# Performance work log

Hardware: AMD Instinct MI355X
Metric: run time of the kernel (lower is better)

Reference implementation:

```python
import jax, jax.numpy as jnp
import numpy as np

QK_DIM = 1024
V_DIM = 1024
NUM_HEADS = 16
HEAD_DIM = 64
INNER = NUM_HEADS * HEAD_DIM  # 1024
SCALE = HEAD_DIM ** -0.5


def setup_inputs() -> dict:
    key = jax.random.key(0)
    ks = jax.random.split(key, 8)
    m, nq, nkv = 4, 2048, 2048
    xq = jax.random.normal(ks[0], (m, nq, QK_DIM), dtype=jnp.float32)
    xk = jax.random.normal(ks[1], (m, nkv, QK_DIM), dtype=jnp.float32)
    xv = jax.random.normal(ks[2], (m, nkv, V_DIM), dtype=jnp.float32)
    # torch nn.Linear weights are [out, in]; y = x @ W.T
    s_qk = (QK_DIM) ** -0.5
    s_in = (INNER) ** -0.5
    Wq = jax.random.uniform(ks[3], (INNER, QK_DIM), jnp.float32, -s_qk, s_qk)
    Wk = jax.random.uniform(ks[4], (INNER, QK_DIM), jnp.float32, -s_qk, s_qk)
    Wv = jax.random.uniform(ks[5], (INNER, V_DIM), jnp.float32, -s_qk, s_qk)
    Wo = jax.random.uniform(ks[6], (V_DIM, INNER), jnp.float32, -s_in, s_in)
    bo = jax.random.uniform(ks[7], (V_DIM,), jnp.float32, -s_in, s_in)
    return {"xq": xq, "xk": xk, "xv": xv, "Wq": Wq, "Wk": Wk, "Wv": Wv, "Wo": Wo, "bo": bo}


def reference(xq, xk, xv, Wq, Wk, Wv, Wo, bo):
    m, nq, _ = xq.shape
    nkv = xk.shape[1]
    # projections (no bias), split heads: b n (h d) -> b h n d
    q = (xq @ Wq.T).reshape(m, nq, NUM_HEADS, HEAD_DIM).transpose(0, 2, 1, 3)
    k = (xk @ Wk.T).reshape(m, nkv, NUM_HEADS, HEAD_DIM).transpose(0, 2, 1, 3)
    v = (xv @ Wv.T).reshape(m, nkv, NUM_HEADS, HEAD_DIM).transpose(0, 2, 1, 3)
    dots = jnp.einsum("bhqd,bhkd->bhqk", q, k) * SCALE  # [m,h,nq,nkv]
    attn = jax.nn.softmax(dots, axis=-1)
    out = jnp.einsum("bhqk,bhkd->bhqd", attn, v)
    out = out.transpose(0, 2, 1, 3).reshape(m, nq, INNER)  # b h n d -> b n (h d)
    return out @ Wo.T + bo  # to_out Linear (dropout p=0 -> identity)
```

## Files before the change

kernel.cpp:

```cpp
#include <hip/hip_runtime.h>

typedef unsigned short u16;
using bf16x8 = __attribute__((ext_vector_type(8))) __bf16;
using f32x4  = __attribute__((ext_vector_type(4))) float;

#define QSCALE 0.18033688011f

#define EXP2F(x) __builtin_amdgcn_exp2f(x)
#define SCHED_FENCE() __builtin_amdgcn_sched_barrier(0)

__device__ __forceinline__ u16 f2bf(float f) {
  union { float f; unsigned int u; } x; x.f = f;
  unsigned int r = x.u + 0x7FFFu + ((x.u >> 16) & 1u);
  return (u16)(r >> 16);
}

__device__ __forceinline__ bf16x8 ld8(const u16* p) {
  return *reinterpret_cast<const bf16x8*>(p);
}

__device__ __forceinline__ void gload16(const void* g, void* l) {
  __builtin_amdgcn_global_load_lds(
      (const __attribute__((address_space(1))) unsigned int*)g,
      (__attribute__((address_space(3))) unsigned int*)l, 16, 0, 0);
}

__global__ void cast4_f32_to_bf16(const float* __restrict__ a, const float* __restrict__ b,
                                  const float* __restrict__ c, const float* __restrict__ d,
                                  u16* __restrict__ out, int n4) {
  const int y = blockIdx.y;
  const int i = blockIdx.x * 256 + threadIdx.x;
  if (i >= n4) return;
  const float* src = (y == 0) ? a : (y == 1) ? b : (y == 2) ? c : d;
  const float4 v = reinterpret_cast<const float4*>(src)[i];
  ushort4 o;
  o.x = f2bf(v.x); o.y = f2bf(v.y); o.z = f2bf(v.z); o.w = f2bf(v.w);
  reinterpret_cast<ushort4*>(out + (size_t)y * n4 * 4)[i] = o;
}

__global__ __launch_bounds__(256)
void gemm_qkv(const float* __restrict__ xq, const float* __restrict__ xk,
              const float* __restrict__ xv, const u16* __restrict__ Ball,
              u16* __restrict__ Call) {
  const int g = (blockIdx.x & 7) * 192 + (blockIdx.x >> 3);
  const int bx = g & 7, by = (g >> 3) & 63, z = g >> 9;
  const float* A = (z == 0) ? xq : (z == 1) ? xk : xv;
  const u16* B = Ball + (size_t)z * 1024 * 1024;
  u16* C = Call + (size_t)z * 8192 * 1024;

  __shared__ alignas(16) float lds_af[128 * 64];
  __shared__ alignas(16) u16 lds_b[128 * 64];
  const int t = threadIdx.x;
  const int w = t >> 6, lane = t & 63;
  const int wr = w >> 1, wc = w & 1;
  const size_t row0 = (size_t)by * 128;
  const size_t col0 = (size_t)bx * 128;

  f32x4 acc[4][4];
#pragma unroll
  for (int i = 0; i < 4; ++i)
#pragma unroll
    for (int j = 0; j < 4; ++j) acc[i][j] = {0.f, 0.f, 0.f, 0.f};

  const int a_r = t >> 4;
  const int a_c = ((t & 15) ^ (a_r & 7)) * 4;
  const float* gaf = A + (row0 + a_r) * 1024 + a_c;
  const int b_r = t >> 3;
  const int b_c = ((t & 7) ^ (b_r & 7)) * 8;
  const u16* gbb = B + (col0 + b_r) * 1024 + b_c;

  const int fr = lane & 15;
  const int flh = lane >> 4;
  const int fx7 = fr & 7;

  for (int kt = 0; kt < 1024; kt += 64) {
    __syncthreads();
#pragma unroll
    for (int s = 0; s < 8; ++s)
      gload16(gaf + (size_t)(16 * s) * 1024 + kt, lds_af + s * 1024 + w * 256);
#pragma unroll
    for (int s = 0; s < 4; ++s)
      gload16(gbb + (size_t)(32 * s) * 1024 + kt, lds_b + s * 2048 + w * 512);
    asm volatile("s_waitcnt vmcnt(0)" ::: "memory");
    __syncthreads();

#pragma unroll
    for (int ks2 = 0; ks2 < 2; ++ks2) {
      bf16x8 af[4], bfr[4];
#pragma unroll
      for (int i = 0; i < 4; ++i) {
        const int row = wr * 64 + i * 16 + fr;
        const int g0 = ks2 * 8 + flh * 2;
        f32x4 lo = *reinterpret_cast<const f32x4*>(&lds_af[row * 64 + ((g0 ^ fx7) << 2)]);
        f32x4 hi = *reinterpret_cast<const f32x4*>(&lds_af[row * 64 + (((g0 + 1) ^ fx7) << 2)]);
        af[i][0] = (__bf16)lo[0]; af[i][1] = (__bf16)lo[1];
        af[i][2] = (__bf16)lo[2]; af[i][3] = (__bf16)lo[3];
        af[i][4] = (__bf16)hi[0]; af[i][5] = (__bf16)hi[1];
        af[i][6] = (__bf16)hi[2]; af[i][7] = (__bf16)hi[3];
      }
#pragma unroll
      for (int j = 0; j < 4; ++j) {
        const int row = wc * 64 + j * 16 + fr;
        const int gch = ks2 * 4 + flh;
        bfr[j] = ld8(&lds_b[row * 64 + ((gch ^ fx7) * 8)]);
      }
#pragma unroll
      for (int i = 0; i < 4; ++i)
#pragma unroll
        for (int j = 0; j < 4; ++j)
          acc[i][j] = __builtin_amdgcn_mfma_f32_16x16x32_bf16(af[i], bfr[j], acc[i][j], 0, 0, 0);
    }
  }

  const int er = (lane >> 4) * 4, ec = lane & 15;
#pragma unroll
  for (int i = 0; i < 4; ++i)
#pragma unroll
    for (int j = 0; j < 4; ++j) {
      const size_t row = row0 + wr * 64 + i * 16 + er;
      const size_t col = col0 + wc * 64 + j * 16 + ec;
      if (z == 0) {
#pragma unroll
        for (int r = 0; r < 4; ++r)
          C[(row + r) * 1024 + col] = f2bf(acc[i][j][r] * QSCALE);
      } else if (z == 1) {
#pragma unroll
        for (int r = 0; r < 4; ++r) {
          const size_t n = row + r;
          const size_t colswz = (col & ~(size_t)63) |
                                ((col & 63) ^ (((n & 7) << 3)));
          C[n * 1024 + colswz] = f2bf(acc[i][j][r]);
        }
      } else {
        ushort4 o4;
        o4.x = f2bf(acc[i][j][0]); o4.y = f2bf(acc[i][j][1]);
        o4.z = f2bf(acc[i][j][2]); o4.w = f2bf(acc[i][j][3]);
        const size_t nloc = row & 2047;
        const size_t d = col & 63;
        size_t pos = (nloc & ~(size_t)31) | (((nloc >> 2) & 3) << 3) |
                     (((nloc >> 4) & 1) << 2) | (nloc & 3);
        pos ^= (d & 7) << 3;
        const size_t idx = (((row >> 11) * 16 + (col >> 6)) * 64 + d) * 2048 + pos;
        *reinterpret_cast<ushort4*>(&C[idx]) = o4;
      }
    }
}

__global__ __launch_bounds__(256)
void gemm_out(const u16* __restrict__ A, const u16* __restrict__ B,
              float* __restrict__ Cf, const float* __restrict__ bias) {
  const int g = (blockIdx.x & 7) * 64 + (blockIdx.x >> 3);
  const int bx = g & 7, by = g >> 3;

  __shared__ alignas(16) u16 lds_a[128 * 64];
  __shared__ alignas(16) u16 lds_b[128 * 64];
  const int t = threadIdx.x;
  const int w = t >> 6, lane = t & 63;
  const int wr = w >> 1, wc = w & 1;
  const size_t row0 = (size_t)by * 128;
  const size_t col0 = (size_t)bx * 128;

  f32x4 acc[4][4];
#pragma unroll
  for (int i = 0; i < 4; ++i)
#pragma unroll
    for (int j = 0; j < 4; ++j) acc[i][j] = {0.f, 0.f, 0.f, 0.f};

  const int b_r = t >> 3;
  const int b_c = ((t & 7) ^ (b_r & 7)) * 8;
  const u16* gaa = A + (row0 + b_r) * 1024 + b_c;
  const u16* gbb = B + (col0 + b_r) * 1024 + b_c;

  const int fr = lane & 15;
  const int flh = lane >> 4;
  const int fx7 = fr & 7;

  for (int kt = 0; kt < 1024; kt += 64) {
    __syncthreads();
#pragma unroll
    for (int s = 0; s < 4; ++s) {
      gload16(gaa + (size_t)(32 * s) * 1024 + kt, lds_a + s * 2048 + w * 512);
      gload16(gbb + (size_t)(32 * s) * 1024 + kt, lds_b + s * 2048 + w * 512);
    }
    asm volatile("s_waitcnt vmcnt(0)" ::: "memory");
    __syncthreads();

#pragma unroll
    for (int ks2 = 0; ks2 < 2; ++ks2) {
      bf16x8 af[4], bfr[4];
      const int gch = ks2 * 4 + flh;
#pragma unroll
      for (int i = 0; i < 4; ++i)
        af[i] = ld8(&lds_a[(wr * 64 + i * 16 + fr) * 64 + ((gch ^ fx7) * 8)]);
#pragma unroll
      for (int j = 0; j < 4; ++j)
        bfr[j] = ld8(&lds_b[(wc * 64 + j * 16 + fr) * 64 + ((gch ^ fx7) * 8)]);
#pragma unroll
      for (int i = 0; i < 4; ++i)
#pragma unroll
        for (int j = 0; j < 4; ++j)
          acc[i][j] = __builtin_amdgcn_mfma_f32_16x16x32_bf16(af[i], bfr[j], acc[i][j], 0, 0, 0);
    }
  }

  const int er = (lane >> 4) * 4, ec = lane & 15;
#pragma unroll
  for (int i = 0; i < 4; ++i)
#pragma unroll
    for (int j = 0; j < 4; ++j) {
      const size_t row = row0 + wr * 64 + i * 16 + er;
      const size_t col = col0 + wc * 64 + j * 16 + ec;
#pragma unroll
      for (int r = 0; r < 4; ++r)
        Cf[(row + r) * 1024 + col] = acc[i][j][r] + bias[col];
    }
}

__global__ __launch_bounds__(512)
void flash_attn(const u16* __restrict__ Q, const u16* __restrict__ Km,
                const u16* __restrict__ Vt, u16* __restrict__ O) {
  const int o_blk = (blockIdx.x & 7) * 64 + (blockIdx.x >> 3);
  const int qt = o_blk & 7, h = (o_blk >> 3) & 15, b = o_blk >> 7;
  const int t = threadIdx.x;
  const int w = t >> 6, lane = t & 63;
  const int l16 = lane & 15, lh = lane >> 4;

  __shared__ alignas(16) u16 kt_lds[2][64][64];
  __shared__ alignas(16) u16 vt_lds[2][64][64];

  const size_t base_qk = ((size_t)b * 2048) * 1024 + (size_t)h * 64;
  const size_t base_vt = ((size_t)(b * 16 + h)) * 64 * 2048;

  bf16x8 qf[2][2];
#pragma unroll
  for (int g = 0; g < 2; ++g) {
    const size_t qrow = (size_t)qt * 256 + (w * 2 + g) * 16 + l16;
    const u16* qp = Q + base_qk + qrow * 1024 + lh * 8;
    qf[g][0] = ld8(qp);
    qf[g][1] = ld8(qp + 32);
  }

  bf16x8 vones;
#pragma unroll
  for (int i = 0; i < 8; ++i) vones[i] = (__bf16)1.0f;

  f32x4 o_acc[2][4];
  f32x4 o_sum[2];
#pragma unroll
  for (int g = 0; g < 2; ++g) {
#pragma unroll
    for (int j = 0; j < 4; ++j) o_acc[g][j] = {0.f, 0.f, 0.f, 0.f};
    o_sum[g] = {0.f, 0.f, 0.f, 0.f};
  }

  const int srow = t >> 3;
  const int schk = (t & 7) * 8;
  const u16* kg = Km + base_qk + (size_t)srow * 1024 + schk;
  const u16* vg = Vt + base_vt + (size_t)srow * 2048 + schk;
  u16* kl0 = &kt_lds[0][0][0] + w * 512;
  u16* kl1 = &kt_lds[1][0][0] + w * 512;
  u16* vl0 = &vt_lds[0][0][0] + w * 512;
  u16* vl1 = &vt_lds[1][0][0] + w * 512;

  gload16(kg, kl0);
  gload16(vg, vl0);

  const int xo = (l16 & 7) << 3;

  for (int it = 0; it < 32; ++it) {
    const int cur = it & 1;
    asm volatile("s_waitcnt vmcnt(0)" ::: "memory");
    SCHED_FENCE();
    __syncthreads();
    SCHED_FENCE();

    if (it != 31) {
      const int nkv = (it + 1) * 64;
      gload16(kg + (size_t)nkv * 1024, cur ? kl0 : kl1);
      gload16(vg + nkv, cur ? vl0 : vl1);
    }
    SCHED_FENCE();

    f32x4 s[2][4];
#pragma unroll
    for (int g = 0; g < 2; ++g)
#pragma unroll
      for (int j = 0; j < 4; ++j) s[g][j] = {0.f, 0.f, 0.f, 0.f};
    __builtin_amdgcn_s_setprio(1);
#pragma unroll
    for (int j = 0; j < 4; ++j)
#pragma unroll
      for (int ks = 0; ks < 2; ++ks) {
        bf16x8 kf = ld8(&kt_lds[cur][j * 16 + l16][(ks * 32 + lh * 8) ^ xo]);
        s[0][j] = __builtin_amdgcn_mfma_f32_16x16x32_bf16(kf, qf[0][ks], s[0][j], 0, 0, 0);
        s[1][j] = __builtin_amdgcn_mfma_f32_16x16x32_bf16(kf, qf[1][ks], s[1][j], 0, 0, 0);
      }
    __builtin_amdgcn_s_setprio(0);

    bf16x8 pa[2][2];
#pragma unroll
    for (int g = 0; g < 2; ++g)
#pragma unroll
      for (int j = 0; j < 4; ++j)
#pragma unroll
        for (int r = 0; r < 4; ++r)
          s[g][j][r] = EXP2F(s[g][j][r]);
#pragma unroll
    for (int g = 0; g < 2; ++g)
#pragma unroll
      for (int c = 0; c < 2; ++c)
#pragma unroll
        for (int i = 0; i < 8; ++i)
          pa[g][c][i] = (__bf16)s[g][2 * c + (i >> 2)][i & 3];

    __builtin_amdgcn_s_setprio(1);
#pragma unroll
    for (int c = 0; c < 2; ++c) {
      o_sum[0] = __builtin_amdgcn_mfma_f32_16x16x32_bf16(pa[0][c], vones, o_sum[0], 0, 0, 0);
      o_sum[1] = __builtin_amdgcn_mfma_f32_16x16x32_bf16(pa[1][c], vones, o_sum[1], 0, 0, 0);
#pragma unroll
      for (int jd = 0; jd < 4; ++jd) {
        bf16x8 vf = ld8(&vt_lds[cur][jd * 16 + l16][(c * 32 + lh * 8) ^ xo]);
        o_acc[0][jd] = __builtin_amdgcn_mfma_f32_16x16x32_bf16(pa[0][c], vf, o_acc[0][jd], 0, 0, 0);
        o_acc[1][jd] = __builtin_amdgcn_mfma_f32_16x16x32_bf16(pa[1][c], vf, o_acc[1][jd], 0, 0, 0);
      }
    }
    __builtin_amdgcn_s_setprio(0);
  }

#pragma unroll
  for (int g = 0; g < 2; ++g) {
    float linv[4];
#pragma unroll
    for (int r = 0; r < 4; ++r) linv[r] = 1.0f / o_sum[g][r];
    const size_t orow0 = (size_t)b * 2048 + (size_t)qt * 256 + (w * 2 + g) * 16;
#pragma unroll
    for (int jd = 0; jd < 4; ++jd) {
      const int col = h * 64 + jd * 16 + l16;
#pragma unroll
      for (int r = 0; r < 4; ++r)
        O[(orow0 + lh * 4 + r) * 1024 + col] = f2bf(o_acc[g][jd][r] * linv[r]);
    }
  }
}

extern "C" void kernel_launch(void* const* d_in, const int* in_sizes, int n_in,
                              void* d_out, int out_size, void* d_ws, size_t ws_size,
                              hipStream_t stream) {
  const float* xq = (const float*)d_in[0];
  const float* xk = (const float*)d_in[1];
  const float* xv = (const float*)d_in[2];
  const float* Wq = (const float*)d_in[3];
  const float* Wk = (const float*)d_in[4];
  const float* Wv = (const float*)d_in[5];
  const float* Wo = (const float*)d_in[6];
  const float* bo = (const float*)d_in[7];
  float* out = (float*)d_out;

  const size_t X = (size_t)8192 * 1024;
  const size_t W = (size_t)1024 * 1024;

  u16* p = (u16*)d_ws;
  u16* attn_bf = p; p += X;
  u16* w_bf  = p; p += 4 * W;
  u16* qkv   = p; p += 3 * X;

  dim3 blk(256);
  cast4_f32_to_bf16<<<dim3(1024, 4), blk, 0, stream>>>(Wq, Wk, Wv, Wo, w_bf, (int)(W / 4));

  gemm_qkv<<<dim3(1536), blk, 0, stream>>>(xq, xk, xv, w_bf, qkv);

  flash_attn<<<dim3(512), dim3(512), 0, stream>>>(qkv, qkv + X, qkv + 2 * X, attn_bf);

  gemm_out<<<dim3(512), blk, 0, stream>>>(attn_bf, w_bf + 3 * W, out, bo);
}
```

Baseline: 176.6 us.

## Double-buffer QKV projection GEMM LDS tiles with K-step of 32

The QKV projection GEMM now uses two LDS buffers with a K tile of 32 instead of one buffer with a K tile of 64. The global-to-LDS loads for the next tile are issued before the MFMAs on the current tile, so memory latency overlaps with compute. This halves the work per iteration and doubles the iteration count while keeping LDS usage the same. The single sync per iteration still waits on vmcnt(0) at the top of each step, which limits how much overlap is possible.

```diff
diff --git a/kernel.cpp b/kernel.cpp
--- a/kernel.cpp
+++ b/kernel.cpp
@@ -48,8 +48,8 @@
   const u16* B = Ball + (size_t)z * 1024 * 1024;
   u16* C = Call + (size_t)z * 8192 * 1024;
 
-  __shared__ alignas(16) float lds_af[128 * 64];
-  __shared__ alignas(16) u16 lds_b[128 * 64];
+  __shared__ alignas(16) float lds_af[2][128 * 32];
+  __shared__ alignas(16) u16 lds_b[2][128 * 32];
   const int t = threadIdx.x;
   const int w = t >> 6, lane = t & 63;
   const int wr = w >> 1, wc = w & 1;
@@ -62,55 +62,62 @@
 #pragma unroll
     for (int j = 0; j < 4; ++j) acc[i][j] = {0.f, 0.f, 0.f, 0.f};
 
-  const int a_r = t >> 4;
-  const int a_c = ((t & 15) ^ (a_r & 7)) * 4;
+  const int a_r = t >> 3;
+  const int a_c = ((t & 7) ^ (a_r & 7)) * 4;
   const float* gaf = A + (row0 + a_r) * 1024 + a_c;
-  const int b_r = t >> 3;
-  const int b_c = ((t & 7) ^ (b_r & 7)) * 8;
+  const int b_r = t >> 2;
+  const int b_c = ((t & 3) ^ (b_r & 3)) * 8;
   const u16* gbb = B + (col0 + b_r) * 1024 + b_c;
 
   const int fr = lane & 15;
   const int flh = lane >> 4;
   const int fx7 = fr & 7;
-
-  for (int kt = 0; kt < 1024; kt += 64) {
+  const int fko = ((flh ^ (fr & 3)) * 8);
+
+#define STAGEQ(tile, buf)                                                          \
+  do {                                                                             \
+    _Pragma("unroll") for (int s = 0; s < 4; ++s)                                  \
+      gload16(gaf + (size_t)(32 * s) * 1024 + (tile) * 32,                         \
+              &lds_af[buf][s * 1024 + w * 256]);                                   \
+    _Pragma("unroll") for (int s = 0; s < 2; ++s)                                  \
+      gload16(gbb + (size_t)(64 * s) * 1024 + (tile) * 32,                         \
+              &lds_b[buf][s * 2048 + w * 512]);                                    \
+  } while (0)
+
+  STAGEQ(0, 0);
+
+  for (int it = 0; it < 32; ++it) {
+    const int cur = it & 1;
+    asm volatile("s_waitcnt vmcnt(0)" ::: "memory");
+    SCHED_FENCE();
     __syncthreads();
-#pragma unroll
-    for (int s = 0; s < 8; ++s)
-      gload16(gaf + (size_t)(16 * s) * 1024 + kt, lds_af + s * 1024 + w * 256);
-#pragma unroll
-    for (int s = 0; s < 4; ++s)
-      gload16(gbb + (size_t)(32 * s) * 1024 + kt, lds_b + s * 2048 + w * 512);
-    asm volatile("s_waitcnt vmcnt(0)" ::: "memory");
-    __syncthreads();
-
-#pragma unroll
-    for (int ks2 = 0; ks2 < 2; ++ks2) {
-      bf16x8 af[4], bfr[4];
-#pragma unroll
-      for (int i = 0; i < 4; ++i) {
-        const int row = wr * 64 + i * 16 + fr;
-        const int g0 = ks2 * 8 + flh * 2;
-        f32x4 lo = *reinterpret_cast<const f32x4*>(&lds_af[row * 64 + ((g0 ^ fx7) << 2)]);
-        f32x4 hi = *reinterpret_cast<const f32x4*>(&lds_af[row * 64 + (((g0 + 1) ^ fx7) << 2)]);
-        af[i][0] = (__bf16)lo[0]; af[i][1] = (__bf16)lo[1];
-        af[i][2] = (__bf16)lo[2]; af[i][3] = (__bf16)lo[3];
-        af[i][4] = (__bf16)hi[0]; af[i][5] = (__bf16)hi[1];
-        af[i][6] = (__bf16)hi[2]; af[i][7] = (__bf16)hi[3];
-      }
-#pragma unroll
-      for (int j = 0; j < 4; ++j) {
-        const int row = wc * 64 + j * 16 + fr;
-        const int gch = ks2 * 4 + flh;
-        bfr[j] = ld8(&lds_b[row * 64 + ((gch ^ fx7) * 8)]);
-      }
-#pragma unroll
-      for (int i = 0; i < 4; ++i)
-#pragma unroll
-        for (int j = 0; j < 4; ++j)
-          acc[i][j] = __builtin_amdgcn_mfma_f32_16x16x32_bf16(af[i], bfr[j], acc[i][j], 0, 0, 0);
-    }
-  }
+    SCHED_FENCE();
+
+    if (it != 31) STAGEQ(it + 1, cur ^ 1);
+    SCHED_FENCE();
+
+    bf16x8 af[4], bfr[4];
+#pragma unroll
+    for (int i = 0; i < 4; ++i) {
+      const int row = wr * 64 + i * 16 + fr;
+      const int g0 = flh * 2;
+      f32x4 lo = *reinterpret_cast<const f32x4*>(&lds_af[cur][row * 32 + ((g0 ^ fx7) << 2)]);
+      f32x4 hi = *reinterpret_cast<const f32x4*>(&lds_af[cur][row * 32 + (((g0 + 1) ^ fx7) << 2)]);
+      af[i][0] = (__bf16)lo[0]; af[i][1] = (__bf16)lo[1];
+      af[i][2] = (__bf16)lo[2]; af[i][3] = (__bf16)lo[3];
+      af[i][4] = (__bf16)hi[0]; af[i][5] = (__bf16)hi[1];
+      af[i][6] = (__bf16)hi[2]; af[i][7] = (__bf16)hi[3];
+    }
+#pragma unroll
+    for (int j = 0; j < 4; ++j)
+      bfr[j] = ld8(&lds_b[cur][(wc * 64 + j * 16 + fr) * 32 + fko]);
+#pragma unroll
+    for (int i = 0; i < 4; ++i)
+#pragma unroll
+      for (int j = 0; j < 4; ++j)
+        acc[i][j] = __builtin_amdgcn_mfma_f32_16x16x32_bf16(af[i], bfr[j], acc[i][j], 0, 0, 0);
+  }
+#undef STAGEQ
 
   const int er = (lane >> 4) * 4, ec = lane & 15;
 #pragma unroll
```

Result: no change. 175.2 us (-0.8%).
